# Kernel tuning notes

Hardware: AMD Instinct MI355X
Metric: run time of the kernel (lower is better)

The kernel has to match this reference:

```python
import jax, jax.numpy as jnp
import numpy as np

TREE_DEPTH = 10
TOTAL = 2 ** (TREE_DEPTH + 1) - 1  # 2047 nodes per tree
G = 64                              # graphs per batch
N = G * TOTAL                       # 131008 nodes
E = 2 * N                           # 262016 directed edges
H = 256                             # h_dim
HALF = H // 2
L = 4                               # num_layers
LABELS = 32
OUT = 32
BN_EPS = 1e-5
LN_EPS = 1e-5


def setup_inputs() -> dict:
    key = jax.random.key(0)
    ks = jax.random.split(key, 16)
    x = jnp.stack([jax.random.randint(ks[0], (N,), 0, TOTAL),
                   jax.random.randint(ks[1], (N,), 0, LABELS)], axis=1)
    edge_src = jax.random.randint(ks[2], (E,), 0, N)
    edge_dst = jax.random.randint(ks[3], (E,), 0, N)
    edge_weight = jax.random.uniform(ks[4], (E,), dtype=jnp.float32)
    batch = jnp.arange(N, dtype=jnp.int64) // TOTAL          # node -> graph id
    root_index = jnp.arange(G, dtype=jnp.int64) * TOTAL      # one root per graph
    s = 0.02
    emb_node = jax.random.normal(ks[5], (TOTAL, HALF), dtype=jnp.float32) * s
    emb_label = jax.random.normal(ks[6], (LABELS, HALF), dtype=jnp.float32) * s
    w = 1.0 / np.sqrt(H)
    W1 = jax.random.normal(ks[7], (L, H, H), dtype=jnp.float32) * w
    b1 = jnp.zeros((L, H), dtype=jnp.float32)
    g1 = jnp.ones((L, H), dtype=jnp.float32)
    be1 = jnp.zeros((L, H), dtype=jnp.float32)
    W2 = jax.random.normal(ks[8], (L, H, H), dtype=jnp.float32) * w
    b2 = jnp.zeros((L, H), dtype=jnp.float32)
    g2 = jnp.ones((L, H), dtype=jnp.float32)
    be2 = jnp.zeros((L, H), dtype=jnp.float32)
    ln_g = jnp.ones((L, H), dtype=jnp.float32)
    ln_b = jnp.zeros((L, H), dtype=jnp.float32)
    Wout = jax.random.normal(ks[9], (OUT, H), dtype=jnp.float32) * w
    return {"x": x, "edge_src": edge_src, "edge_dst": edge_dst,
            "edge_weight": edge_weight, "batch": batch, "root_index": root_index,
            "emb_node": emb_node, "emb_label": emb_label,
            "W1": W1, "b1": b1, "g1": g1, "be1": be1,
            "W2": W2, "b2": b2, "g2": g2, "be2": be2,
            "ln_g": ln_g, "ln_b": ln_b, "Wout": Wout}


def _batchnorm(h, g, b):
    # BatchNorm1d, training-mode batch statistics over the node dim
    m = h.mean(axis=0)
    v = h.var(axis=0)
    return g * (h - m) * jax.lax.rsqrt(v + BN_EPS) + b


def _layernorm(h, g, b):
    m = h.mean(axis=-1, keepdims=True)
    v = h.var(axis=-1, keepdims=True)
    return g * (h - m) * jax.lax.rsqrt(v + LN_EPS) + b


def reference(x, edge_src, edge_dst, edge_weight, batch, root_index,
              emb_node, emb_label, W1, b1, g1, be1, W2, b2, g2, be2,
              ln_g, ln_b, Wout):
    # BiEmbedding_cat: concat of two h/2 embeddings
    h = jnp.concatenate([emb_node[x[:, 0]], emb_label[x[:, 1]]], axis=-1)  # [N,H]
    target_roots = root_index[batch]  # all-nodes->root targets for last layer
    for i in range(L):
        if i == L - 1:  # last_layer_fully_adjacent: every node sends to its root
            agg = jnp.zeros_like(h).at[target_roots].add(h)
        else:
            agg = jnp.zeros_like(h).at[edge_dst].add(h[edge_src] * edge_weight[:, None])
        m = h + agg  # GIN with eps=0: (1+eps)*x + sum_j w_ij x_j
        m = jax.nn.relu(_batchnorm(m @ W1[i].T + b1[i], g1[i], be1[i]))
        m = jax.nn.relu(_batchnorm(m @ W2[i].T + b2[i], g2[i], be2[i]))
        # use_activation: relu (idempotent after the MLP's trailing relu)
        h = h + m  # use_residual
        h = _layernorm(h, ln_g[i], ln_b[i])
    roots_x = h[root_index]  # [G,H] root readout
    return roots_x @ Wout.T  # [G,OUT], bias-free out layer
```

## Files before the change

kernel.cpp:

```cpp
#include <hip/hip_runtime.h>
#include <stdint.h>

#define NN 131008
#define NPAD 131072
#define EE 262016
#define HD 256
#define GG 64
#define TT 2047

typedef __attribute__((ext_vector_type(8))) short bfrag;
typedef __attribute__((ext_vector_type(4))) float f32x4;

__device__ __forceinline__ float bflo(unsigned u){ union{unsigned i; float f;} v; v.i = u<<16; return v.f; }
__device__ __forceinline__ float bfhi(unsigned u){ union{unsigned i; float f;} v; v.i = u & 0xffff0000u; return v.f; }
__device__ __forceinline__ unsigned short f2bf(float f){
  union{unsigned i; float fl;} v; v.fl = f; unsigned i = v.i;
  return (unsigned short)((i + 0x7fffu + ((i>>16)&1u)) >> 16);
}
__device__ __forceinline__ unsigned pack2(float a, float b){
  return (unsigned)f2bf(a) | ((unsigned)f2bf(b)<<16);
}
__device__ __forceinline__ void gload16(const void* g, void* s){
  __builtin_amdgcn_global_load_lds((__attribute__((address_space(1))) void*)g,
                                   (__attribute__((address_space(3))) void*)s, 16, 0, 0);
}

__device__ __forceinline__ short bnrelu1(short t, float a, float c){
  union{unsigned i; float f;} v; v.i = ((unsigned)(unsigned short)t) << 16;
  return (short)f2bf(fmaxf(a*v.f + c, 0.f));
}
__device__ __forceinline__ bfrag bn8(bfrag t, float4 a0, float4 a1, float4 c0, float4 c1){
  bfrag r;
  r[0]=bnrelu1(t[0],a0.x,c0.x); r[1]=bnrelu1(t[1],a0.y,c0.y);
  r[2]=bnrelu1(t[2],a0.z,c0.z); r[3]=bnrelu1(t[3],a0.w,c0.w);
  r[4]=bnrelu1(t[4],a1.x,c1.x); r[5]=bnrelu1(t[5],a1.y,c1.y);
  r[6]=bnrelu1(t[6],a1.z,c1.z); r[7]=bnrelu1(t[7],a1.w,c1.w);
  return r;
}

__device__ __forceinline__ void atomic_add_bf16x2(unsigned short* p, float a, float b){
#if __has_builtin(__builtin_amdgcn_global_atomic_fadd_v2bf16)
  typedef __attribute__((ext_vector_type(2))) short s16x2;
  s16x2 v; v.x = (short)f2bf(a); v.y = (short)f2bf(b);
  __builtin_amdgcn_global_atomic_fadd_v2bf16((__attribute__((address_space(1))) s16x2*)p, v);
#else
  unsigned* up = (unsigned*)p;
  unsigned old = *up, assumed;
  do {
    assumed = old;
    unsigned nv = pack2(bflo(assumed) + a, bfhi(assumed) + b);
    old = atomicCAS(up, assumed, nv);
  } while (old != assumed);
#endif
}

__global__ void k_prep(const float* __restrict__ W1, const float* __restrict__ W2,
                       unsigned short* __restrict__ wbf,
                       const int* __restrict__ x, const float* __restrict__ en,
                       const float* __restrict__ el, unsigned short* __restrict__ hbf,
                       const int* __restrict__ ed, int* __restrict__ deg){
  int b = blockIdx.x;
  if (b < 2048){
    int idx = b*256 + threadIdx.x;
    float v = (idx < 262144) ? W1[idx] : W2[idx - 262144];
    wbf[idx] = f2bf(v);
  } else if (b < 18432){
    size_t i8 = ((size_t)(b - 2048)*256 + threadIdx.x) << 3;
    int row = (int)(i8 >> 8); int k = (int)(i8 & 255);
    uint4 o;
    if (row < NN){
      const float* src = (k < 128) ? en + (size_t)x[2*row]*128 + k
                                   : el + (size_t)x[2*row+1]*128 + (k-128);
      float4 v0 = *(const float4*)src;
      float4 v1 = *(const float4*)(src + 4);
      o.x = pack2(v0.x, v0.y); o.y = pack2(v0.z, v0.w);
      o.z = pack2(v1.x, v1.y); o.w = pack2(v1.z, v1.w);
    } else { o.x = o.y = o.z = o.w = 0u; }
    *(uint4*)(hbf + i8) = o;
  } else {
    int e = (b - 18432)*256 + threadIdx.x;
    if (e < EE) atomicAdd(&deg[ed[e]], 1);
  }
}

__global__ void k_scan_block(const int* __restrict__ deg, int* __restrict__ start,
                             int* __restrict__ bsum){
  __shared__ int sh[256];
  int t = threadIdx.x;
  int i = blockIdx.x*256 + t;
  int v = deg[i];
  int val = v; sh[t] = val; __syncthreads();
  for (int off = 1; off < 256; off <<= 1){
    int add = (t >= off) ? sh[t-off] : 0;
    __syncthreads();
    val += add; sh[t] = val;
    __syncthreads();
  }
  start[i] = val - v;
  if (t == 255) bsum[blockIdx.x] = val;
}
__global__ void k_scan_top(int* __restrict__ bsum){
  __shared__ int sh[512];
  int t = threadIdx.x;
  int v = bsum[t];
  int val = v; sh[t] = val; __syncthreads();
  for (int off = 1; off < 512; off <<= 1){
    int add = (t >= off) ? sh[t-off] : 0;
    __syncthreads();
    val += add; sh[t] = val;
    __syncthreads();
  }
  bsum[t] = val - v;
}
__global__ void k_fill(const int* __restrict__ es, const int* __restrict__ ed,
                       const float* __restrict__ ew, const int* __restrict__ start,
                       const int* __restrict__ bsum,
                       int* __restrict__ cursor0, uint2* __restrict__ pairs){
  int e = blockIdx.x*256 + threadIdx.x;
  if (e < EE){
    int d = ed[e];
    int pos = start[d] + bsum[d >> 8] + atomicAdd(&cursor0[d], 1);
    uint2 p; p.x = (unsigned)es[e];
    union{float f; unsigned u;} w; w.f = ew[e];
    p.y = w.u;
    pairs[pos] = p;
  }
}

__global__ void k_gather(const int* __restrict__ deg, const int* __restrict__ start,
                         const int* __restrict__ bsum,
                         const uint2* __restrict__ pairs,
                         const unsigned short* __restrict__ hbf,
                         unsigned short* __restrict__ mbf){
  int half = threadIdx.x >> 5, lane32 = threadIdx.x & 31;
  int row = blockIdx.x*8 + half;
  size_t base = (size_t)row*HD + (lane32 << 3);
  uint4 o;
  if (row < NN){
    uint4 hv = *(const uint4*)(hbf + base);
    float a0 = bflo(hv.x), a1 = bfhi(hv.x), a2 = bflo(hv.y), a3 = bfhi(hv.y);
    float a4 = bflo(hv.z), a5 = bfhi(hv.z), a6 = bflo(hv.w), a7 = bfhi(hv.w);
    int d = deg[row], s = start[row] + bsum[row >> 8];
    for (int j = 0; j < d; ++j){
      uint2 pr = pairs[s + j];
      union{unsigned u; float f;} wg; wg.u = pr.y;
      uint4 sv = *(const uint4*)(hbf + (size_t)pr.x*HD + (lane32 << 3));
      a0 += bflo(sv.x)*wg.f; a1 += bfhi(sv.x)*wg.f;
      a2 += bflo(sv.y)*wg.f; a3 += bfhi(sv.y)*wg.f;
      a4 += bflo(sv.z)*wg.f; a5 += bfhi(sv.z)*wg.f;
      a6 += bflo(sv.w)*wg.f; a7 += bfhi(sv.w)*wg.f;
    }
    o.x = pack2(a0, a1); o.y = pack2(a2, a3);
    o.z = pack2(a4, a5); o.w = pack2(a6, a7);
  } else { o.x = o.y = o.z = o.w = 0u; }
  *(uint4*)(mbf + base) = o;
}

__global__ void k_rootsum(const unsigned short* __restrict__ hbf, unsigned short* __restrict__ m){
  int g = blockIdx.x >> 4, ch = blockIdx.x & 15;
  int col = threadIdx.x * 2;
  int nr = (ch == 15) ? 127 : 128;
  const unsigned short* p = hbf + ((size_t)g*TT + ch*128)*HD + col;
  float a = 0.f, b = 0.f;
  for (int r = 0; r < nr; ++r){
    unsigned u = *(const unsigned*)(p + (size_t)r*HD);
    a += bflo(u); b += bfhi(u);
  }
  atomic_add_bf16x2(m + (size_t)g*TT*HD + col, a, b);
}

template<bool TRANS>
__device__ __forceinline__ void gemm_body(const unsigned short* __restrict__ A,
                                          const unsigned short* __restrict__ B,
                                          unsigned short* __restrict__ C,
                                          float* __restrict__ gsum, float* __restrict__ gsq,
                                          const float* __restrict__ sum1,
                                          const float* __restrict__ sq1,
                                          const float* __restrict__ g1v,
                                          const float* __restrict__ be1v){
  __shared__ unsigned short Bs[65536];
  __shared__ float st[512];
  __shared__ float acf[256];
  __shared__ float ccf[256];
  const int tid = threadIdx.x, lane = tid & 63, w = tid >> 6;
  const int wr = w >> 1, wc = w & 1;
  const int b = blockIdx.x;
  const int q = lane >> 4, r15 = lane & 15, r7 = lane & 7;

  if (TRANS && tid < 256){
    const float inv_n = 1.f/(float)NN;
    float mean = sum1[tid] * inv_n;
    float var  = fmaxf(sq1[tid] * inv_n - mean*mean, 0.f);
    float aj   = g1v[tid] * rsqrtf(var + 1e-5f);
    acf[tid] = aj;
    ccf[tid] = be1v[tid] - aj*mean;
  }
  st[tid < 512 ? tid : 0] = 0.f;

#pragma unroll
  for (int kt = 0; kt < 4; ++kt)
#pragma unroll
    for (int it = 0; it < 4; ++it){
      int ci = it*512 + tid;
      int row = ci >> 3, cp = ci & 7;
      int cl = cp ^ (row & 7);
      gload16(B + (size_t)row*HD + kt*64 + cl*8, &Bs[kt*16384 + ci*8]);
    }

  bfrag rA[4][2];
  auto aload = [&](int s, int slot){
    const int t2 = b*4 + (s >> 3), ks = s & 7;
    const unsigned short* p = A + ((size_t)(t2*128 + wr*32 + r15))*HD + ks*32 + (q << 3);
    rA[slot][0] = *(const bfrag*)p;
    rA[slot][1] = *(const bfrag*)(p + 16*HD);
  };
  aload(0, 0); aload(1, 1); aload(2, 2);

  asm volatile("s_waitcnt vmcnt(0) lgkmcnt(0)" ::: "memory");
  __builtin_amdgcn_s_barrier();

  f32x4 acc[2][8];
  f32x4 zz = {0.f, 0.f, 0.f, 0.f};
#pragma unroll
  for (int a = 0; a < 2; ++a)
#pragma unroll
    for (int c = 0; c < 8; ++c) acc[a][c] = zz;
  float cs[8] = {0,0,0,0,0,0,0,0}, cq[8] = {0,0,0,0,0,0,0,0};

#pragma unroll 4
  for (int s = 0; s < 32; ++s){
    if (s < 29) aload(s + 3, (s + 3) & 3);

    bfrag a0 = rA[s & 3][0], a1 = rA[s & 3][1];
    const int ks = s & 7;
    if (TRANS){
      const int kb = ks*32 + (q << 3);
      float4 ca0 = *(const float4*)&acf[kb];
      float4 ca1 = *(const float4*)&acf[kb + 4];
      float4 cc0 = *(const float4*)&ccf[kb];
      float4 cc1 = *(const float4*)&ccf[kb + 4];
      a0 = bn8(a0, ca0, ca1, cc0, cc1);
      a1 = bn8(a1, ca0, ca1, cc0, cc1);
    }

    const int kt64 = ks >> 1, hf = ks & 1;
    bfrag bf[8];
#pragma unroll
    for (int ct = 0; ct < 8; ++ct){
      int rb = wc*128 + ct*16 + r15;
      bf[ct] = *(const bfrag*)&Bs[kt64*16384 + rb*64 + (((q + 4*hf) ^ r7) << 3)];
    }
    __builtin_amdgcn_s_setprio(1);
#pragma unroll
    for (int ct = 0; ct < 8; ++ct){
      acc[0][ct] = __builtin_amdgcn_mfma_f32_16x16x32_bf16(a0, bf[ct], acc[0][ct], 0, 0, 0);
      acc[1][ct] = __builtin_amdgcn_mfma_f32_16x16x32_bf16(a1, bf[ct], acc[1][ct], 0, 0, 0);
    }
    __builtin_amdgcn_s_setprio(0);

    if ((s & 7) == 7){
      const int tile = b*4 + (s >> 3);
      const int lr0 = wr*32 + q*4;
      const int lc0 = wc*128 + r15;
#pragma unroll
      for (int rt = 0; rt < 2; ++rt)
#pragma unroll
        for (int ct = 0; ct < 8; ++ct){
#pragma unroll
          for (int i = 0; i < 4; ++i){
            size_t grow = (size_t)tile*128 + lr0 + rt*16 + i;
            float v = acc[rt][ct][i];
            C[grow*HD + lc0 + ct*16] = f2bf(v);
            if (grow < NN){ cs[ct] += v; cq[ct] += v*v; }
          }
          acc[rt][ct] = zz;
        }
    }
  }

  const int lc0 = wc*128 + r15;
#pragma unroll
  for (int ct = 0; ct < 8; ++ct){
    float s2 = cs[ct], q2 = cq[ct];
    s2 += __shfl_xor(s2, 16); s2 += __shfl_xor(s2, 32);
    q2 += __shfl_xor(q2, 16); q2 += __shfl_xor(q2, 32);
    if (q == 0){
      atomicAdd(&st[lc0 + ct*16], s2);
      atomicAdd(&st[256 + lc0 + ct*16], q2);
    }
  }
  __syncthreads();
  if (tid < 256){
    atomicAdd(&gsum[tid], st[tid]);
    atomicAdd(&gsq[tid], st[256 + tid]);
  }
}

__global__ __launch_bounds__(512) void k_gemm(const unsigned short* __restrict__ A,
                                              const unsigned short* __restrict__ B,
                                              unsigned short* __restrict__ C,
                                              float* __restrict__ gsum, float* __restrict__ gsq){
  gemm_body<false>(A, B, C, gsum, gsq, nullptr, nullptr, nullptr, nullptr);
}
__global__ __launch_bounds__(512) void k_gemm2(const unsigned short* __restrict__ T,
                                               const float* __restrict__ sum1,
                                               const float* __restrict__ sq1,
                                               const float* __restrict__ g1v,
                                               const float* __restrict__ be1v,
                                               const unsigned short* __restrict__ B,
                                               unsigned short* __restrict__ C,
                                               float* __restrict__ gsum, float* __restrict__ gsq){
  gemm_body<true>(T, B, C, gsum, gsq, sum1, sq1, g1v, be1v);
}

__device__ __forceinline__ void coef4(float4 s4, float4 q4, float4 g4, float4 b4,
                                      float4& a, float4& c){
  const float inv_n = 1.f/(float)NN;
  float m0 = s4.x*inv_n, m1 = s4.y*inv_n, m2 = s4.z*inv_n, m3 = s4.w*inv_n;
  float i0 = rsqrtf(fmaxf(q4.x*inv_n - m0*m0, 0.f) + 1e-5f);
  float i1 = rsqrtf(fmaxf(q4.y*inv_n - m1*m1, 0.f) + 1e-5f);
  float i2 = rsqrtf(fmaxf(q4.z*inv_n - m2*m2, 0.f) + 1e-5f);
  float i3 = rsqrtf(fmaxf(q4.w*inv_n - m3*m3, 0.f) + 1e-5f);
  a.x = g4.x*i0; a.y = g4.y*i1; a.z = g4.z*i2; a.w = g4.w*i3;
  c.x = b4.x - a.x*m0; c.y = b4.y - a.y*m1; c.z = b4.z - a.z*m2; c.w = b4.w - a.w*m3;
}

__global__ void k_fuse(const unsigned short* t2,
                       const float* __restrict__ sum, const float* __restrict__ sq,
                       const float* __restrict__ g, const float* __restrict__ be,
                       const float* __restrict__ lg, const float* __restrict__ lb,
                       unsigned short* __restrict__ hbf, unsigned short* mbf,
                       int writem){
  int half = threadIdx.x >> 5, lane32 = threadIdx.x & 31;
  size_t row = (size_t)blockIdx.x*8 + half;
  int col = lane32 << 3;
  size_t base = row*HD + col;
  uint4 o;
  if (row < NN){
    float4 av0, cv0, av1, cv1;
    coef4(*(const float4*)(sum + col),     *(const float4*)(sq + col),
          *(const float4*)(g + col),       *(const float4*)(be + col),     av0, cv0);
    coef4(*(const float4*)(sum + col + 4), *(const float4*)(sq + col + 4),
          *(const float4*)(g + col + 4),   *(const float4*)(be + col + 4), av1, cv1);
    uint4 tv = *(const uint4*)(t2 + base);
    uint4 hv = *(const uint4*)(hbf + base);
    float r0 = bflo(hv.x) + fmaxf(av0.x*bflo(tv.x) + cv0.x, 0.f);
    float r1 = bfhi(hv.x) + fmaxf(av0.y*bfhi(tv.x) + cv0.y, 0.f);
    float r2 = bflo(hv.y) + fmaxf(av0.z*bflo(tv.y) + cv0.z, 0.f);
    float r3 = bfhi(hv.y) + fmaxf(av0.w*bfhi(tv.y) + cv0.w, 0.f);
    float r4 = bflo(hv.z) + fmaxf(av1.x*bflo(tv.z) + cv1.x, 0.f);
    float r5 = bfhi(hv.z) + fmaxf(av1.y*bfhi(tv.z) + cv1.y, 0.f);
    float r6 = bflo(hv.w) + fmaxf(av1.z*bflo(tv.w) + cv1.z, 0.f);
    float r7 = bfhi(hv.w) + fmaxf(av1.w*bfhi(tv.w) + cv1.w, 0.f);
    float s  = r0+r1+r2+r3+r4+r5+r6+r7;
    float qq = r0*r0+r1*r1+r2*r2+r3*r3+r4*r4+r5*r5+r6*r6+r7*r7;
#pragma unroll
    for (int d = 1; d < 32; d <<= 1){ s += __shfl_xor(s, d); qq += __shfl_xor(qq, d); }
    float mean = s * (1.f/256.f);
    float var  = fmaxf(qq * (1.f/256.f) - mean*mean, 0.f);
    float inv  = rsqrtf(var + 1e-5f);
    float4 gv0 = *(const float4*)(lg + col), gv1 = *(const float4*)(lg + col + 4);
    float4 bv0 = *(const float4*)(lb + col), bv1 = *(const float4*)(lb + col + 4);
    o.x = pack2(gv0.x*(r0 - mean)*inv + bv0.x, gv0.y*(r1 - mean)*inv + bv0.y);
    o.y = pack2(gv0.z*(r2 - mean)*inv + bv0.z, gv0.w*(r3 - mean)*inv + bv0.w);
    o.z = pack2(gv1.x*(r4 - mean)*inv + bv1.x, gv1.y*(r5 - mean)*inv + bv1.y);
    o.w = pack2(gv1.z*(r6 - mean)*inv + bv1.z, gv1.w*(r7 - mean)*inv + bv1.w);
  } else {
    o.x = o.y = o.z = o.w = 0u;
  }
  *(uint4*)(hbf + base) = o;
  if (writem) *(uint4*)(mbf + base) = o;
}

__global__ void k_readout(const unsigned short* __restrict__ hbf, const float* __restrict__ Wo,
                          float* __restrict__ out){
  int g = blockIdx.x;
  int w = threadIdx.x >> 6, lane = threadIdx.x & 63;
  uint2 hv = *(const uint2*)(hbf + (size_t)g*TT*HD + (lane<<2));
  float h0 = bflo(hv.x), h1 = bfhi(hv.x), h2 = bflo(hv.y), h3 = bfhi(hv.y);
#pragma unroll
  for (int oo = 0; oo < 8; ++oo){
    int o = w*8 + oo;
    float4 wv = *(const float4*)(Wo + (size_t)o*HD + (lane<<2));
    float p = h0*wv.x + h1*wv.y + h2*wv.z + h3*wv.w;
#pragma unroll
    for (int d = 1; d < 64; d <<= 1) p += __shfl_xor(p, d);
    if (lane == 0) out[g*32 + o] = p;
  }
}

extern "C" void kernel_launch(void* const* d_in, const int* in_sizes, int n_in,
                              void* d_out, int out_size, void* d_ws, size_t ws_size,
                              hipStream_t stream){
  const int*   x   = (const int*)d_in[0];
  const int*   es  = (const int*)d_in[1];
  const int*   ed  = (const int*)d_in[2];
  const float* ew  = (const float*)d_in[3];
  const float* en  = (const float*)d_in[6];
  const float* el  = (const float*)d_in[7];
  const float* W1  = (const float*)d_in[8];
  const float* g1  = (const float*)d_in[10];
  const float* be1 = (const float*)d_in[11];
  const float* W2  = (const float*)d_in[12];
  const float* g2  = (const float*)d_in[14];
  const float* be2 = (const float*)d_in[15];
  const float* lg  = (const float*)d_in[16];
  const float* lb  = (const float*)d_in[17];
  const float* Wo  = (const float*)d_in[18];

  char* ws = (char*)d_ws;
  unsigned short* hbf = (unsigned short*)ws;
  unsigned short* mbf = (unsigned short*)(ws + 67108864);
  unsigned short* t   = (unsigned short*)(ws + 134217728);
  unsigned short* wbf = (unsigned short*)(ws + 201326592);
  float* stats   = (float*)(ws + 202375168);
  int*   deg     = (int*)  (ws + 202391552);
  int*   cursor0 = (int*)  (ws + 202915840);
  int*   start   = (int*)  (ws + 203440128);
  int*   bsum    = (int*)  (ws + 203964416);
  uint2* pairs   = (uint2*)(ws + 203968512);

  hipMemsetAsync(stats, 0, 16384 + 524288 + 524288, stream);
  k_prep<<<19456, 256, 0, stream>>>(W1, W2, wbf, x, en, el, hbf, ed, deg);

  k_scan_block<<<512, 256, 0, stream>>>(deg, start, bsum);
  k_scan_top  <<<1,   512, 0, stream>>>(bsum);
  k_fill      <<<1024,256, 0, stream>>>(es, ed, ew, start, bsum, cursor0, pairs);

  for (int i = 0; i < 4; ++i){
    float* s1 = stats + (2*i)*512;
    float* s2 = stats + (2*i+1)*512;
    if (i < 3) k_gather <<<16384, 256, 0, stream>>>(deg, start, bsum, pairs, hbf, mbf);
    else       k_rootsum<<<1024,  128, 0, stream>>>(hbf, mbf);

    k_gemm <<<256, 512, 0, stream>>>(mbf, wbf + i*65536, t, s1, s1 + 256);
    k_gemm2<<<256, 512, 0, stream>>>(t, s1, s1 + 256, g1 + i*256, be1 + i*256,
                                     wbf + 262144 + i*65536, mbf, s2, s2 + 256);
    k_fuse <<<16384, 256, 0, stream>>>(mbf, s2, s2 + 256, g2 + i*256, be2 + i*256,
                                       lg + i*256, lb + i*256, hbf, mbf, (i == 2) ? 1 : 0);
  }

  k_readout<<<64, 256, 0, stream>>>(hbf, Wo, (float*)d_out);
  (void)in_sizes; (void)n_in; (void)out_size; (void)ws_size;
}
```

Measured before the change: 754.3 us.

## Fuse both MLP GEMMs into one kernel with grid-wide barrier for BN stats

Replaces the two GEMM kernels with one persistent-style kernel. The first GEMM's output stays in registers as packed bf16, a global atomic counter acts as a grid barrier so the first BatchNorm statistics are complete, and then BN plus ReLU are applied while staging into LDS for the second GEMM. This removes the write and re-read of the intermediate tensor and one launch. The cost is many live registers (tpk arrays), W staged in halves, and a spin barrier that assumes all 256 blocks are co-resident. The gather loop is also unrolled by two so two neighbour loads are in flight at once.

```diff
diff --git a/kernel.cpp b/kernel.cpp
--- a/kernel.cpp
+++ b/kernel.cpp
@@ -23,19 +23,6 @@
 __device__ __forceinline__ void gload16(const void* g, void* s){
   __builtin_amdgcn_global_load_lds((__attribute__((address_space(1))) void*)g,
                                    (__attribute__((address_space(3))) void*)s, 16, 0, 0);
-}
-
-__device__ __forceinline__ short bnrelu1(short t, float a, float c){
-  union{unsigned i; float f;} v; v.i = ((unsigned)(unsigned short)t) << 16;
-  return (short)f2bf(fmaxf(a*v.f + c, 0.f));
-}
-__device__ __forceinline__ bfrag bn8(bfrag t, float4 a0, float4 a1, float4 c0, float4 c1){
-  bfrag r;
-  r[0]=bnrelu1(t[0],a0.x,c0.x); r[1]=bnrelu1(t[1],a0.y,c0.y);
-  r[2]=bnrelu1(t[2],a0.z,c0.z); r[3]=bnrelu1(t[3],a0.w,c0.w);
-  r[4]=bnrelu1(t[4],a1.x,c1.x); r[5]=bnrelu1(t[5],a1.y,c1.y);
-  r[6]=bnrelu1(t[6],a1.z,c1.z); r[7]=bnrelu1(t[7],a1.w,c1.w);
-  return r;
 }
 
 __device__ __forceinline__ void atomic_add_bf16x2(unsigned short* p, float a, float b){
@@ -141,7 +128,20 @@
     float a0 = bflo(hv.x), a1 = bfhi(hv.x), a2 = bflo(hv.y), a3 = bfhi(hv.y);
     float a4 = bflo(hv.z), a5 = bfhi(hv.z), a6 = bflo(hv.w), a7 = bfhi(hv.w);
     int d = deg[row], s = start[row] + bsum[row >> 8];
-    for (int j = 0; j < d; ++j){
+    int j = 0;
+    for (; j + 2 <= d; j += 2){
+      uint2 p0 = pairs[s + j];
+      uint2 p1 = pairs[s + j + 1];
+      union{unsigned u; float f;} w0; w0.u = p0.y;
+      union{unsigned u; float f;} w1; w1.u = p1.y;
+      uint4 s0 = *(const uint4*)(hbf + (size_t)p0.x*HD + (lane32 << 3));
+      uint4 s1 = *(const uint4*)(hbf + (size_t)p1.x*HD + (lane32 << 3));
+      a0 += bflo(s0.x)*w0.f + bflo(s1.x)*w1.f; a1 += bfhi(s0.x)*w0.f + bfhi(s1.x)*w1.f;
+      a2 += bflo(s0.y)*w0.f + bflo(s1.y)*w1.f; a3 += bfhi(s0.y)*w0.f + bfhi(s1.y)*w1.f;
+      a4 += bflo(s0.z)*w0.f + bflo(s1.z)*w1.f; a5 += bfhi(s0.z)*w0.f + bfhi(s1.z)*w1.f;
+      a6 += bflo(s0.w)*w0.f + bflo(s1.w)*w1.f; a7 += bfhi(s0.w)*w0.f + bfhi(s1.w)*w1.f;
+    }
+    if (j < d){
       uint2 pr = pairs[s + j];
       union{unsigned u; float f;} wg; wg.u = pr.y;
       uint4 sv = *(const uint4*)(hbf + (size_t)pr.x*HD + (lane32 << 3));
@@ -169,148 +169,244 @@
   atomic_add_bf16x2(m + (size_t)g*TT*HD + col, a, b);
 }
 
-template<bool TRANS>
-__device__ __forceinline__ void gemm_body(const unsigned short* __restrict__ A,
-                                          const unsigned short* __restrict__ B,
-                                          unsigned short* __restrict__ C,
-                                          float* __restrict__ gsum, float* __restrict__ gsq,
-                                          const float* __restrict__ sum1,
-                                          const float* __restrict__ sq1,
-                                          const float* __restrict__ g1v,
-                                          const float* __restrict__ be1v){
-  __shared__ unsigned short Bs[65536];
-  __shared__ float st[512];
+__global__ __launch_bounds__(512) void k_gemmf(
+    unsigned short* AB,
+    const unsigned short* __restrict__ W1b,
+    const unsigned short* __restrict__ W2b,
+    const float* __restrict__ g1v, const float* __restrict__ be1v,
+    float* __restrict__ s1sum, float* __restrict__ s1sq,
+    float* __restrict__ s2sum, float* __restrict__ s2sq,
+    int* __restrict__ ctr){
+  __shared__ unsigned short Ws[32768];
+  __shared__ unsigned short tb[32768];
   __shared__ float acf[256];
   __shared__ float ccf[256];
+  __shared__ float st[512];
   const int tid = threadIdx.x, lane = tid & 63, w = tid >> 6;
   const int wr = w >> 1, wc = w & 1;
   const int b = blockIdx.x;
   const int q = lane >> 4, r15 = lane & 15, r7 = lane & 7;
 
-  if (TRANS && tid < 256){
+  st[tid >= 512 ? 0 : tid] = 0.f;
+
+  unsigned tpk[4][2][2][4][2];
+
+  auto stageW = [&](const unsigned short* Wsrc){
+#pragma unroll
+    for (int kt = 0; kt < 4; ++kt)
+#pragma unroll
+      for (int it = 0; it < 2; ++it){
+        int ci = it*512 + tid;
+        int row = ci >> 3, cp = ci & 7;
+        int cl = cp ^ (row & 7);
+        gload16(Wsrc + (size_t)row*HD + kt*64 + cl*8, &Ws[kt*8192 + ci*8]);
+      }
+  };
+
+  bfrag rA[4][2];
+  auto aload = [&](int s, int slot){
+    const unsigned short* p = AB + ((size_t)((b*4 + (s >> 3))*128 + wr*32 + r15))*HD
+                                 + (s & 7)*32 + (q << 3);
+    rA[slot][0] = *(const bfrag*)p;
+    rA[slot][1] = *(const bfrag*)(p + 16*HD);
+  };
+
+  f32x4 zz = {0.f, 0.f, 0.f, 0.f};
+
+#pragma unroll
+  for (int h = 0; h < 2; ++h){
+    __syncthreads();
+    stageW(W1b + (size_t)h*128*HD);
+    aload(0, 0); aload(1, 1); aload(2, 2);
+    asm volatile("s_waitcnt vmcnt(0) lgkmcnt(0)" ::: "memory");
+    __builtin_amdgcn_s_barrier();
+    __builtin_amdgcn_sched_barrier(0);
+
+    f32x4 acc[2][4];
+#pragma unroll
+    for (int a = 0; a < 2; ++a)
+#pragma unroll
+      for (int c = 0; c < 4; ++c) acc[a][c] = zz;
+    float cs1[4] = {0.f,0.f,0.f,0.f}, cq1[4] = {0.f,0.f,0.f,0.f};
+
+#pragma unroll
+    for (int tile = 0; tile < 4; ++tile){
+#pragma unroll
+      for (int kc = 0; kc < 8; ++kc){
+        const int s = tile*8 + kc;
+        if (s < 29) aload(s + 3, (s + 3) & 3);
+        const bfrag a0 = rA[s & 3][0], a1 = rA[s & 3][1];
+        __builtin_amdgcn_s_setprio(1);
+#pragma unroll
+        for (int ct = 0; ct < 4; ++ct){
+          bfrag bf = *(const bfrag*)&Ws[(kc >> 1)*8192 + (wc*64 + ct*16 + r15)*64
+                                        + (((q + 4*(kc & 1)) ^ r7) << 3)];
+          acc[0][ct] = __builtin_amdgcn_mfma_f32_16x16x32_bf16(a0, bf, acc[0][ct], 0, 0, 0);
+          acc[1][ct] = __builtin_amdgcn_mfma_f32_16x16x32_bf16(a1, bf, acc[1][ct], 0, 0, 0);
+        }
+        __builtin_amdgcn_s_setprio(0);
+      }
+#pragma unroll
+      for (int rt = 0; rt < 2; ++rt)
+#pragma unroll
+        for (int ct = 0; ct < 4; ++ct){
+#pragma unroll
+          for (int i = 0; i < 4; ++i){
+            size_t grow = (size_t)(b*4 + tile)*128 + wr*32 + rt*16 + q*4 + i;
+            float v = acc[rt][ct][i];
+            if (grow < NN){ cs1[ct] += v; cq1[ct] += v*v; }
+          }
+          tpk[tile][h][rt][ct][0] = pack2(acc[rt][ct][0], acc[rt][ct][1]);
+          tpk[tile][h][rt][ct][1] = pack2(acc[rt][ct][2], acc[rt][ct][3]);
+          acc[rt][ct] = zz;
+        }
+    }
+#pragma unroll
+    for (int ct = 0; ct < 4; ++ct){
+      float sv = cs1[ct], qv = cq1[ct];
+      sv += __shfl_xor(sv, 16); sv += __shfl_xor(sv, 32);
+      qv += __shfl_xor(qv, 16); qv += __shfl_xor(qv, 32);
+      if (q == 0){
+        int col = h*128 + wc*64 + ct*16 + r15;
+        atomicAdd(&st[col], sv);
+        atomicAdd(&st[256 + col], qv);
+      }
+    }
+  }
+
+  __syncthreads();
+  if (tid < 256){
+    atomicAdd(&s1sum[tid], st[tid]);
+    atomicAdd(&s1sq[tid],  st[256 + tid]);
+  }
+  __threadfence();
+  __syncthreads();
+  if (tid == 0){
+    __hip_atomic_fetch_add(ctr, 1, __ATOMIC_ACQ_REL, __HIP_MEMORY_SCOPE_AGENT);
+    for (int spin = 0; spin < (1 << 20); ++spin){
+      if (__hip_atomic_load(ctr, __ATOMIC_ACQUIRE, __HIP_MEMORY_SCOPE_AGENT) >= (int)gridDim.x)
+        break;
+      __builtin_amdgcn_s_sleep(8);
+    }
+  }
+  __syncthreads();
+
+  if (tid < 256){
     const float inv_n = 1.f/(float)NN;
-    float mean = sum1[tid] * inv_n;
-    float var  = fmaxf(sq1[tid] * inv_n - mean*mean, 0.f);
+    float s  = __hip_atomic_load(&s1sum[tid], __ATOMIC_RELAXED, __HIP_MEMORY_SCOPE_AGENT);
+    float qq = __hip_atomic_load(&s1sq[tid],  __ATOMIC_RELAXED, __HIP_MEMORY_SCOPE_AGENT);
+    float mean = s * inv_n;
+    float var  = fmaxf(qq * inv_n - mean*mean, 0.f);
     float aj   = g1v[tid] * rsqrtf(var + 1e-5f);
     acf[tid] = aj;
     ccf[tid] = be1v[tid] - aj*mean;
   }
-  st[tid < 512 ? tid : 0] = 0.f;
-
-#pragma unroll
-  for (int kt = 0; kt < 4; ++kt)
-#pragma unroll
-    for (int it = 0; it < 4; ++it){
-      int ci = it*512 + tid;
-      int row = ci >> 3, cp = ci & 7;
-      int cl = cp ^ (row & 7);
-      gload16(B + (size_t)row*HD + kt*64 + cl*8, &Bs[kt*16384 + ci*8]);
-    }
-
-  bfrag rA[4][2];
-  auto aload = [&](int s, int slot){
-    const int t2 = b*4 + (s >> 3), ks = s & 7;
-    const unsigned short* p = A + ((size_t)(t2*128 + wr*32 + r15))*HD + ks*32 + (q << 3);
-    rA[slot][0] = *(const bfrag*)p;
-    rA[slot][1] = *(const bfrag*)(p + 16*HD);
-  };
-  aload(0, 0); aload(1, 1); aload(2, 2);
-
-  asm volatile("s_waitcnt vmcnt(0) lgkmcnt(0)" ::: "memory");
-  __builtin_amdgcn_s_barrier();
-
-  f32x4 acc[2][8];
-  f32x4 zz = {0.f, 0.f, 0.f, 0.f};
-#pragma unroll
-  for (int a = 0; a < 2; ++a)
-#pragma unroll
-    for (int c = 0; c < 8; ++c) acc[a][c] = zz;
-  float cs[8] = {0,0,0,0,0,0,0,0}, cq[8] = {0,0,0,0,0,0,0,0};
-
-#pragma unroll 4
-  for (int s = 0; s < 32; ++s){
-    if (s < 29) aload(s + 3, (s + 3) & 3);
-
-    bfrag a0 = rA[s & 3][0], a1 = rA[s & 3][1];
-    const int ks = s & 7;
-    if (TRANS){
-      const int kb = ks*32 + (q << 3);
-      float4 ca0 = *(const float4*)&acf[kb];
-      float4 ca1 = *(const float4*)&acf[kb + 4];
-      float4 cc0 = *(const float4*)&ccf[kb];
-      float4 cc1 = *(const float4*)&ccf[kb + 4];
-      a0 = bn8(a0, ca0, ca1, cc0, cc1);
-      a1 = bn8(a1, ca0, ca1, cc0, cc1);
-    }
-
-    const int kt64 = ks >> 1, hf = ks & 1;
-    bfrag bf[8];
-#pragma unroll
-    for (int ct = 0; ct < 8; ++ct){
-      int rb = wc*128 + ct*16 + r15;
-      bf[ct] = *(const bfrag*)&Bs[kt64*16384 + rb*64 + (((q + 4*hf) ^ r7) << 3)];
-    }
-    __builtin_amdgcn_s_setprio(1);
-#pragma unroll
-    for (int ct = 0; ct < 8; ++ct){
-      acc[0][ct] = __builtin_amdgcn_mfma_f32_16x16x32_bf16(a0, bf[ct], acc[0][ct], 0, 0, 0);
-      acc[1][ct] = __builtin_amdgcn_mfma_f32_16x16x32_bf16(a1, bf[ct], acc[1][ct], 0, 0, 0);
-    }
-    __builtin_amdgcn_s_setprio(0);
-
-    if ((s & 7) == 7){
-      const int tile = b*4 + (s >> 3);
-      const int lr0 = wr*32 + q*4;
-      const int lc0 = wc*128 + r15;
-#pragma unroll
-      for (int rt = 0; rt < 2; ++rt)
-#pragma unroll
-        for (int ct = 0; ct < 8; ++ct){
+  st[tid >= 512 ? 0 : tid] = 0.f;
+  __syncthreads();
+
+  float ac[8], cc[8];
+#pragma unroll
+  for (int h = 0; h < 2; ++h)
+#pragma unroll
+    for (int ct = 0; ct < 4; ++ct){
+      int col = h*128 + wc*64 + ct*16 + r15;
+      ac[h*4 + ct] = acf[col];
+      cc[h*4 + ct] = ccf[col];
+    }
+
+  char* tbc = (char*)tb;
+#pragma unroll
+  for (int h2 = 0; h2 < 2; ++h2){
+    __syncthreads();
+    stageW(W2b + (size_t)h2*128*HD);
+    asm volatile("s_waitcnt vmcnt(0)" ::: "memory");
+    __builtin_amdgcn_s_barrier();
+    __builtin_amdgcn_sched_barrier(0);
+
+    float cs2[4] = {0.f,0.f,0.f,0.f}, cq2[4] = {0.f,0.f,0.f,0.f};
+#pragma unroll
+    for (int tile = 0; tile < 4; ++tile){
+      if (tile){
+        asm volatile("s_waitcnt lgkmcnt(0)" ::: "memory");
+        __builtin_amdgcn_s_barrier();
+        __builtin_amdgcn_sched_barrier(0);
+      }
+#pragma unroll
+      for (int h = 0; h < 2; ++h)
+#pragma unroll
+        for (int rt = 0; rt < 2; ++rt)
+#pragma unroll
+          for (int ct = 0; ct < 4; ++ct)
+#pragma unroll
+            for (int pr = 0; pr < 2; ++pr){
+              unsigned u = tpk[tile][h][rt][ct][pr];
+              float aa = ac[h*4 + ct], cv = cc[h*4 + ct];
+              int col  = h*128 + wc*64 + ct*16 + r15;
+              int row0 = wr*32 + rt*16 + q*4 + pr*2;
+              unsigned short b0 = f2bf(fmaxf(aa*bflo(u) + cv, 0.f));
+              unsigned short b1 = f2bf(fmaxf(aa*bfhi(u) + cv, 0.f));
+              *(unsigned short*)(tbc + row0*512 + ((((col >> 3) ^ (row0 & 7)) << 4)) + ((col & 7) << 1)) = b0;
+              *(unsigned short*)(tbc + (row0+1)*512 + ((((col >> 3) ^ ((row0+1) & 7)) << 4)) + ((col & 7) << 1)) = b1;
+            }
+      asm volatile("s_waitcnt lgkmcnt(0)" ::: "memory");
+      __builtin_amdgcn_s_barrier();
+      __builtin_amdgcn_sched_barrier(0);
+
+      f32x4 acc2[2][4];
+#pragma unroll
+      for (int a = 0; a < 2; ++a)
+#pragma unroll
+        for (int c = 0; c < 4; ++c) acc2[a][c] = zz;
+
+      __builtin_amdgcn_s_setprio(1);
+#pragma unroll
+      for (int kc = 0; kc < 8; ++kc){
+        bfrag af2[2];
+#pragma unroll
+        for (int rt2 = 0; rt2 < 2; ++rt2){
+          int row = wr*32 + rt2*16 + r15;
+          af2[rt2] = *(const bfrag*)(tbc + row*512 + ((((kc << 2) | q) ^ r7) << 4));
+        }
+#pragma unroll
+        for (int ct = 0; ct < 4; ++ct){
+          bfrag bf2 = *(const bfrag*)&Ws[(kc >> 1)*8192 + (wc*64 + ct*16 + r15)*64
+                                         + (((q + 4*(kc & 1)) ^ r7) << 3)];
+          acc2[0][ct] = __builtin_amdgcn_mfma_f32_16x16x32_bf16(af2[0], bf2, acc2[0][ct], 0, 0, 0);
+          acc2[1][ct] = __builtin_amdgcn_mfma_f32_16x16x32_bf16(af2[1], bf2, acc2[1][ct], 0, 0, 0);
+        }
+      }
+      __builtin_amdgcn_s_setprio(0);
+
+#pragma unroll
+      for (int rt2 = 0; rt2 < 2; ++rt2)
+#pragma unroll
+        for (int ct = 0; ct < 4; ++ct){
 #pragma unroll
           for (int i = 0; i < 4; ++i){
-            size_t grow = (size_t)tile*128 + lr0 + rt*16 + i;
-            float v = acc[rt][ct][i];
-            C[grow*HD + lc0 + ct*16] = f2bf(v);
-            if (grow < NN){ cs[ct] += v; cq[ct] += v*v; }
+            size_t grow = (size_t)(b*4 + tile)*128 + wr*32 + rt2*16 + q*4 + i;
+            float v = acc2[rt2][ct][i];
+            AB[grow*HD + h2*128 + wc*64 + ct*16 + r15] = f2bf(v);
+            if (grow < NN){ cs2[ct] += v; cq2[ct] += v*v; }
           }
-          acc[rt][ct] = zz;
         }
     }
-  }
-
-  const int lc0 = wc*128 + r15;
-#pragma unroll
-  for (int ct = 0; ct < 8; ++ct){
-    float s2 = cs[ct], q2 = cq[ct];
-    s2 += __shfl_xor(s2, 16); s2 += __shfl_xor(s2, 32);
-    q2 += __shfl_xor(q2, 16); q2 += __shfl_xor(q2, 32);
-    if (q == 0){
-      atomicAdd(&st[lc0 + ct*16], s2);
-      atomicAdd(&st[256 + lc0 + ct*16], q2);
+#pragma unroll
+    for (int ct = 0; ct < 4; ++ct){
+      float sv = cs2[ct], qv = cq2[ct];
+      sv += __shfl_xor(sv, 16); sv += __shfl_xor(sv, 32);
+      qv += __shfl_xor(qv, 16); qv += __shfl_xor(qv, 32);
+      if (q == 0){
+        int col = h2*128 + wc*64 + ct*16 + r15;
+        atomicAdd(&st[col], sv);
+        atomicAdd(&st[256 + col], qv);
+      }
     }
   }
   __syncthreads();
   if (tid < 256){
-    atomicAdd(&gsum[tid], st[tid]);
-    atomicAdd(&gsq[tid], st[256 + tid]);
-  }
-}
-
-__global__ __launch_bounds__(512) void k_gemm(const unsigned short* __restrict__ A,
-                                              const unsigned short* __restrict__ B,
-                                              unsigned short* __restrict__ C,
-                                              float* __restrict__ gsum, float* __restrict__ gsq){
-  gemm_body<false>(A, B, C, gsum, gsq, nullptr, nullptr, nullptr, nullptr);
-}
-__global__ __launch_bounds__(512) void k_gemm2(const unsigned short* __restrict__ T,
-                                               const float* __restrict__ sum1,
-                                               const float* __restrict__ sq1,
-                                               const float* __restrict__ g1v,
-                                               const float* __restrict__ be1v,
-                                               const unsigned short* __restrict__ B,
-                                               unsigned short* __restrict__ C,
-                                               float* __restrict__ gsum, float* __restrict__ gsq){
-  gemm_body<true>(T, B, C, gsum, gsq, sum1, sq1, g1v, be1v);
+    atomicAdd(&s2sum[tid], st[tid]);
+    atomicAdd(&s2sq[tid],  st[256 + tid]);
+  }
 }
 
 __device__ __forceinline__ void coef4(float4 s4, float4 q4, float4 g4, float4 b4,
@@ -411,7 +507,7 @@
   char* ws = (char*)d_ws;
   unsigned short* hbf = (unsigned short*)ws;
   unsigned short* mbf = (unsigned short*)(ws + 67108864);
-  unsigned short* t   = (unsigned short*)(ws + 134217728);
+  int*   ctr    = (int*)  (ws + 134217728);
   unsigned short* wbf = (unsigned short*)(ws + 201326592);
   float* stats   = (float*)(ws + 202375168);
   int*   deg     = (int*)  (ws + 202391552);
@@ -421,6 +517,7 @@
   uint2* pairs   = (uint2*)(ws + 203968512);
 
   hipMemsetAsync(stats, 0, 16384 + 524288 + 524288, stream);
+  hipMemsetAsync(ctr, 0, 16, stream);
   k_prep<<<19456, 256, 0, stream>>>(W1, W2, wbf, x, en, el, hbf, ed, deg);
 
   k_scan_block<<<512, 256, 0, stream>>>(deg, start, bsum);
@@ -433,9 +530,9 @@
     if (i < 3) k_gather <<<16384, 256, 0, stream>>>(deg, start, bsum, pairs, hbf, mbf);
     else       k_rootsum<<<1024,  128, 0, stream>>>(hbf, mbf);
 
-    k_gemm <<<256, 512, 0, stream>>>(mbf, wbf + i*65536, t, s1, s1 + 256);
-    k_gemm2<<<256, 512, 0, stream>>>(t, s1, s1 + 256, g1 + i*256, be1 + i*256,
-                                     wbf + 262144 + i*65536, mbf, s2, s2 + 256);
+    k_gemmf<<<256, 512, 0, stream>>>(mbf, wbf + i*65536, wbf + 262144 + i*65536,
+                                     g1 + i*256, be1 + i*256,
+                                     s1, s1 + 256, s2, s2 + 256, ctr + i);
     k_fuse <<<16384, 256, 0, stream>>>(mbf, s2, s2 + 256, g2 + i*256, be2 + i*256,
                                        lg + i*256, lb + i*256, hbf, mbf, (i == 2) ? 1 : 0);
   }
```

New measurement: 1.923 ms. 155% more time.
